# Kernel optimization log

Hardware: AMD Instinct MI355X
Metric: run time of the kernel (lower is better)

## Reference

```python
import jax, jax.numpy as jnp
import numpy as np

SHIFT = 1  # fixed value of the module's random shift_direction (+1 or -1)


def setup_inputs() -> dict:
    key = jax.random.key(0)
    k1, k2 = jax.random.split(key)
    x = jax.random.normal(k1, (128, 128, 56, 56), dtype=jnp.float32)  # [N, C_in, H, W]
    w = jax.random.normal(k2, (32, 128, 3), dtype=jnp.float32)        # [C_out, C_in, K]
    return {"x": x, "w": w}


def reference(x, w):
    # The original unfold+einsum is a 1D conv over W (kernel 3, pad 1), identity over H.
    # y[m,j,n,l] = sum_{i,k} x[m,i,n,l+k-1] * w[j,i,k]  (zero-padded)
    kern = w[:, :, None, :]  # [C_out, C_in, 1, 3] -> OIHW
    y = jax.lax.conv_general_dilated(
        x, kern,
        window_strides=(1, 1),
        padding=((0, 0), (1, 1)),
        dimension_numbers=("NCHW", "OIHW", "NCHW"),
    )  # [128, 32, 56, 56]
    # The reshape/permute/roll/permute chain == circular shift along the H axis.
    return jnp.roll(y, SHIFT, axis=2)
```

## Files before the change

### kernel.cpp

```cpp
#include <hip/hip_runtime.h>


#define NB    128
#define CIN   128
#define SP    3136
#define OUTC  32
#define ST    126
#define NT    25
#define ROWS  128
#define CP    136
#define THREADS 256

typedef __attribute__((ext_vector_type(8)))  short bf16x8;
typedef __attribute__((ext_vector_type(16))) float f32x16;

__device__ __forceinline__ unsigned short f2bf(float f) {
    unsigned u = __float_as_uint(f);
    return (unsigned short)((u + 0x7FFFu + ((u >> 16) & 1u)) >> 16);
}
__device__ __forceinline__ unsigned pack2bf(float a, float b) {
    return (unsigned)f2bf(a) | ((unsigned)f2bf(b) << 16);
}

__global__ void prep_w(const float* __restrict__ w, unsigned short* __restrict__ af) {
    int i = blockIdx.x * 256 + threadIdx.x;
    if (i >= OUTC * 384) return;
    int k = i % 384, o = i / 384;
    int tap = k / 128, c = k % 128;
    int kstep = k >> 4, klocal = k & 15;
    int lane  = ((klocal >> 3) << 5) + o;
    int j     = klocal & 7;
    af[kstep * 512 + lane * 8 + j] = f2bf(w[o * 384 + c * 3 + tap]);
}

__launch_bounds__(THREADS, 4)
__global__ void conv_mfma(const float* __restrict__ x,
                          const unsigned short* __restrict__ af,
                          float* __restrict__ out) {
    __shared__ unsigned short xs[ROWS * CP];

    const int n  = blockIdx.y;
    const int s0 = blockIdx.x * ST;
    const float* __restrict__ xn = x + (size_t)n * (CIN * SP);

#pragma unroll
    for (int it = 0; it < 8; ++it) {
        int i  = threadIdx.x + it * THREADS;
        int j  = i & (ROWS - 1);
        int cg = i >> 7;
        int sp = s0 - 1 + j;
        sp = sp < 0 ? 0 : (sp > SP - 1 ? SP - 1 : sp);
        const float* __restrict__ xp = xn + (size_t)(cg * 8) * SP + sp;
        float v0 = xp[0 * SP], v1 = xp[1 * SP], v2 = xp[2 * SP], v3 = xp[3 * SP];
        float v4 = xp[4 * SP], v5 = xp[5 * SP], v6 = xp[6 * SP], v7 = xp[7 * SP];
        union { unsigned u[4]; bf16x8 v; } pk;
        pk.u[0] = pack2bf(v0, v1);
        pk.u[1] = pack2bf(v2, v3);
        pk.u[2] = pack2bf(v4, v5);
        pk.u[3] = pack2bf(v6, v7);
        *(bf16x8*)&xs[j * CP + cg * 8] = pk.v;
    }
    __syncthreads();

    const int lane  = threadIdx.x & 63;
    const int wid   = threadIdx.x >> 6;
    const int cloc  = wid * 32 + (lane & 31);
    const int col   = s0 + cloc;
    const int wpos  = col % 56;
    const int half  = lane >> 5;

    f32x16 acc;
#pragma unroll
    for (int r = 0; r < 16; ++r) acc[r] = 0.0f;

#pragma unroll
    for (int tap = 0; tap < 3; ++tap) {
        int jrow = cloc + tap;
        if (jrow > ROWS - 1) jrow = ROWS - 1;
        const unsigned short* brow = &xs[jrow * CP + half * 8];
        const bool kill = (tap == 0 && wpos == 0) || (tap == 2 && wpos == 55);
#pragma unroll
        for (int ks8 = 0; ks8 < 8; ++ks8) {
            bf16x8 b = *(const bf16x8*)(brow + ks8 * 16);
            if (kill) {
#pragma unroll
                for (int t = 0; t < 8; ++t) b[t] = 0;
            }
            const bf16x8 a = *(const bf16x8*)(af + (tap * 8 + ks8) * 512 + lane * 8);
            acc = __builtin_amdgcn_mfma_f32_32x32x16_bf16(a, b, acc, 0, 0, 0);
        }
    }

    if (cloc < ST && col < SP) {
        int sst = col + 56;
        if (sst >= SP) sst -= SP;
        float* op = out + (size_t)n * (OUTC * SP) + sst;
#pragma unroll
        for (int r = 0; r < 16; ++r) {
            int o = (r & 3) + 8 * (r >> 2) + 4 * half;
            op[o * SP] = acc[r];
        }
    }
}

extern "C" void kernel_launch(void* const* d_in, const int* in_sizes, int n_in,
                              void* d_out, int out_size, void* d_ws, size_t ws_size,
                              hipStream_t stream) {
    const float* x = (const float*)d_in[0];
    const float* w = (const float*)d_in[1];
    float* out = (float*)d_out;
    unsigned short* af = (unsigned short*)d_ws;

    prep_w<<<dim3((OUTC * 384 + 255) / 256), dim3(256), 0, stream>>>(w, af);

    dim3 grid(NT, NB);
    conv_mfma<<<grid, dim3(THREADS), 0, stream>>>(x, af, out);
}
```

Before: 307.3 us.

## Load input as float2 pairs, use zero row for padding, nontemporal stores

The input staging loop now reads pairs of adjacent spatial positions as float2, which halves the load instructions, and packs them with the hardware bf16x2 conversion. The staging tile is realigned to an even start, so the tile step shrinks to 122 and the grid grows to 26 tiles. Boundary taps now point at a shared zero row in LDS instead of masking B fragments in registers. Output stores become nontemporal. These changes target load instruction count and register-side masking, at the cost of slightly more tiles with redundant halo work.

Result: no change. 309.5 us (+0.7%).

```diff
diff --git a/kernel.cpp b/kernel.cpp
--- a/kernel.cpp
+++ b/kernel.cpp
@@ -1,13 +1,16 @@
 #include <hip/hip_runtime.h>
+#include <hip/hip_bf16.h>
 
 
 #define NB    128
 #define CIN   128
 #define SP    3136
+#define HSP   1568
 #define OUTC  32
-#define ST    126
-#define NT    25
+#define ST    122
+#define NT    26
 #define ROWS  128
+#define ZROW  128
 #define CP    136
 #define THREADS 256
 
@@ -18,8 +21,11 @@
     unsigned u = __float_as_uint(f);
     return (unsigned short)((u + 0x7FFFu + ((u >> 16) & 1u)) >> 16);
 }
-__device__ __forceinline__ unsigned pack2bf(float a, float b) {
-    return (unsigned)f2bf(a) | ((unsigned)f2bf(b) << 16);
+
+__device__ __forceinline__ unsigned cvt2(float a, float b) {
+    union { __hip_bfloat162 h; unsigned u; } z;
+    z.h = __float22bfloat162_rn(make_float2(a, b));
+    return z.u;
 }
 
 __global__ void prep_w(const float* __restrict__ w, unsigned short* __restrict__ af) {
@@ -37,37 +43,44 @@
 __global__ void conv_mfma(const float* __restrict__ x,
                           const unsigned short* __restrict__ af,
                           float* __restrict__ out) {
-    __shared__ unsigned short xs[ROWS * CP];
+    __shared__ unsigned short xs[(ROWS + 1) * CP];
 
     const int n  = blockIdx.y;
     const int s0 = blockIdx.x * ST;
     const float* __restrict__ xn = x + (size_t)n * (CIN * SP);
 
+    if (threadIdx.x < 16) {
+        bf16x8 z = {};
+        *(bf16x8*)&xs[ZROW * CP + threadIdx.x * 8] = z;
+    }
+
 #pragma unroll
-    for (int it = 0; it < 8; ++it) {
+    for (int it = 0; it < 4; ++it) {
         int i  = threadIdx.x + it * THREADS;
-        int j  = i & (ROWS - 1);
-        int cg = i >> 7;
-        int sp = s0 - 1 + j;
-        sp = sp < 0 ? 0 : (sp > SP - 1 ? SP - 1 : sp);
-        const float* __restrict__ xp = xn + (size_t)(cg * 8) * SP + sp;
-        float v0 = xp[0 * SP], v1 = xp[1 * SP], v2 = xp[2 * SP], v3 = xp[3 * SP];
-        float v4 = xp[4 * SP], v5 = xp[5 * SP], v6 = xp[6 * SP], v7 = xp[7 * SP];
-        union { unsigned u[4]; bf16x8 v; } pk;
-        pk.u[0] = pack2bf(v0, v1);
-        pk.u[1] = pack2bf(v2, v3);
-        pk.u[2] = pack2bf(v4, v5);
-        pk.u[3] = pack2bf(v6, v7);
-        *(bf16x8*)&xs[j * CP + cg * 8] = pk.v;
+        int p  = i & 63;
+        int cg = i >> 6;
+        int s  = s0 - 2 + 2 * p;
+        s = s < 0 ? 0 : (s > SP - 2 ? SP - 2 : s);
+        const float2* __restrict__ xp =
+            (const float2*)xn + (size_t)(cg * 8) * HSP + (s >> 1);
+        float2 v0 = xp[0 * HSP], v1 = xp[1 * HSP], v2 = xp[2 * HSP], v3 = xp[3 * HSP];
+        float2 v4 = xp[4 * HSP], v5 = xp[5 * HSP], v6 = xp[6 * HSP], v7 = xp[7 * HSP];
+        union { unsigned u[4]; bf16x8 v; } r0, r1;
+        r0.u[0] = cvt2(v0.x, v1.x); r0.u[1] = cvt2(v2.x, v3.x);
+        r0.u[2] = cvt2(v4.x, v5.x); r0.u[3] = cvt2(v6.x, v7.x);
+        r1.u[0] = cvt2(v0.y, v1.y); r1.u[1] = cvt2(v2.y, v3.y);
+        r1.u[2] = cvt2(v4.y, v5.y); r1.u[3] = cvt2(v6.y, v7.y);
+        *(bf16x8*)&xs[(2 * p)     * CP + cg * 8] = r0.v;
+        *(bf16x8*)&xs[(2 * p + 1) * CP + cg * 8] = r1.v;
     }
     __syncthreads();
 
-    const int lane  = threadIdx.x & 63;
-    const int wid   = threadIdx.x >> 6;
-    const int cloc  = wid * 32 + (lane & 31);
-    const int col   = s0 + cloc;
-    const int wpos  = col % 56;
-    const int half  = lane >> 5;
+    const int lane = threadIdx.x & 63;
+    const int wid  = threadIdx.x >> 6;
+    const int cloc = wid * 32 + (lane & 31);
+    const int col  = s0 + cloc;
+    const int wpos = col % 56;
+    const int half = lane >> 5;
 
     f32x16 acc;
 #pragma unroll
@@ -75,17 +88,14 @@
 
 #pragma unroll
     for (int tap = 0; tap < 3; ++tap) {
-        int jrow = cloc + tap;
+        int jrow = cloc + tap + 1;
         if (jrow > ROWS - 1) jrow = ROWS - 1;
+        if ((tap == 0 && wpos == 0) || (tap == 2 && wpos == 55))
+            jrow = ZROW;
         const unsigned short* brow = &xs[jrow * CP + half * 8];
-        const bool kill = (tap == 0 && wpos == 0) || (tap == 2 && wpos == 55);
 #pragma unroll
         for (int ks8 = 0; ks8 < 8; ++ks8) {
             bf16x8 b = *(const bf16x8*)(brow + ks8 * 16);
-            if (kill) {
-#pragma unroll
-                for (int t = 0; t < 8; ++t) b[t] = 0;
-            }
             const bf16x8 a = *(const bf16x8*)(af + (tap * 8 + ks8) * 512 + lane * 8);
             acc = __builtin_amdgcn_mfma_f32_32x32x16_bf16(a, b, acc, 0, 0, 0);
         }
@@ -98,7 +108,7 @@
 #pragma unroll
         for (int r = 0; r < 16; ++r) {
             int o = (r & 3) + 8 * (r >> 2) + 4 * half;
-            op[o * SP] = acc[r];
+            __builtin_nontemporal_store(acc[r], op + o * SP);
         }
     }
 }
```
